# Kernel optimization log

Measured on AMD Instinct MI355X. Metric: run time of the kernel, lower is better.

## Reference

```python
import jax, jax.numpy as jnp
import numpy as np

CHANNELS = 256
N_HEADS = 8
WS = 8
HEAD_DIM = CHANNELS // N_HEADS
SCALE = HEAD_DIM ** -0.5
EPS = 1e-5


def setup_inputs() -> dict:
    key = jax.random.key(0)
    ks = jax.random.split(key, 7)
    C = CHANNELS
    B, T, H, W = 2, 4, 64, 64
    x = jax.random.normal(ks[0], (B * T, C, H, W), dtype=jnp.float32)
    s = 1.0 / np.sqrt(C)
    w_qkv = jax.random.uniform(ks[1], (3 * C, C), jnp.float32, -s, s)
    b_qkv = jax.random.uniform(ks[2], (3 * C,), jnp.float32, -s, s)
    w_proj = jax.random.uniform(ks[3], (C, C), jnp.float32, -s, s)
    b_proj = jax.random.uniform(ks[4], (C,), jnp.float32, -s, s)
    gamma = jnp.ones((C,), jnp.float32)
    beta = jnp.zeros((C,), jnp.float32)
    return {"x": x, "w_qkv": w_qkv, "b_qkv": b_qkv, "w_proj": w_proj,
            "b_proj": b_proj, "gamma": gamma, "beta": beta, "T": T}


def _forward(x, w_qkv, b_qkv, w_proj, b_proj, gamma, beta, T):
    BT, C, H, W = x.shape
    B = BT // T
    ws = WS
    pH = (ws - H % ws) % ws
    pW = (ws - W % ws) % ws
    if pH > 0 or pW > 0:
        x_p = jnp.pad(x, ((0, 0), (0, 0), (0, pH), (0, pW)))
    else:
        x_p = x
    Hp, Wp = H + pH, W + pW
    nH, nW = Hp // ws, Wp // ws
    # partition: (B,T,C,nH,ws,nW,ws) -> (B,nH,nW,T,ws,ws,C) -> (B*nH*nW, T*ws*ws, C)
    xw = x_p.reshape(B, T, C, nH, ws, nW, ws)
    xw = jnp.transpose(xw, (0, 3, 5, 1, 4, 6, 2))
    L = T * ws * ws
    xw = xw.reshape(B * nH * nW, L, C)
    # LayerNorm over channels
    mu = jnp.mean(xw, axis=-1, keepdims=True)
    var = jnp.mean(jnp.square(xw - mu), axis=-1, keepdims=True)
    xn = (xw - mu) * jax.lax.rsqrt(var + EPS) * gamma + beta
    # QKV projection
    qkv = xn @ w_qkv.T + b_qkv  # (NW, L, 3C)
    qkv = qkv.reshape(xw.shape[0], L, 3, N_HEADS, HEAD_DIM)
    q, k, v = qkv[:, :, 0], qkv[:, :, 1], qkv[:, :, 2]  # (NW, L, h, d)
    scores = jnp.einsum('nlhd,nmhd->nhlm', q, k) * SCALE
    attn = jax.nn.softmax(scores, axis=-1)
    out = jnp.einsum('nhlm,nmhd->nlhd', attn, v).reshape(xw.shape[0], L, C)
    out = out @ w_proj.T + b_proj
    out = xw + out
    # unpartition
    out = out.reshape(B, nH, nW, T, ws, ws, C)
    out = jnp.transpose(out, (0, 3, 6, 1, 4, 2, 5)).reshape(B * T, C, Hp, Wp)
    if pH > 0 or pW > 0:
        out = out[:, :, :H, :W]
    return out


def reference(x, w_qkv, b_qkv, w_proj, b_proj, gamma, beta, T):
    return _forward(x, w_qkv, b_qkv, w_proj, b_proj, gamma, beta, T)
```

## Files before the change

### kernel.cpp

```cpp
#include <hip/hip_runtime.h>
#include <hip/hip_bf16.h>

typedef __hip_bfloat16 bf16;
typedef __attribute__((ext_vector_type(8))) short short8;
typedef __attribute__((ext_vector_type(4))) short sh4;
typedef __attribute__((ext_vector_type(4))) float f32x4;

#define SCALE_F 0.17677669529663687f
#define LOG2E_F 1.4426950408889634f
#define EPS_F 1e-5f
#define NW_CHUNK 32
#define ROWS_CHUNK (NW_CHUNK * 256)

#define OW_QKV  0
#define OW_PROJ 196608
#define OB_QKV  262144
#define OB_PROJ 262912
#define NWB     263168

__device__ __forceinline__ float b2f(bf16 v) { return __bfloat162float(v); }
__device__ __forceinline__ bf16 f2b(float v) { return __float2bfloat16(v); }
__device__ __forceinline__ short f2bs(float v) { bf16 h = f2b(v); return *(short*)&h; }
__device__ __forceinline__ float bs2f(short s) { bf16 h = *(bf16*)&s; return __bfloat162float(h); }

__device__ __forceinline__ float ldin(const void* p, size_t i, int mode) {
  if (mode) return ((const float*)p)[i];
  return b2f(((const bf16*)p)[i]);
}
__device__ __forceinline__ void stout(void* p, size_t i, int mode, float v) {
  if (mode) ((float*)p)[i] = v;
  else      ((bf16*)p)[i] = f2b(v);
}
__device__ __forceinline__ float4 ldin4(const void* p, size_t i, int mode) {
  if (mode) return *(const float4*)((const float*)p + i);
  const sh4 s = *(const sh4*)((const short*)p + i);
  return make_float4(bs2f(s[0]), bs2f(s[1]), bs2f(s[2]), bs2f(s[3]));
}

__device__ __forceinline__ void gld16(void* lds, const void* g) {
  __builtin_amdgcn_global_load_lds(
      (const __attribute__((address_space(1))) unsigned int*)g,
      (__attribute__((address_space(3))) unsigned int*)lds, 16, 0, 0);
}

__global__ __launch_bounds__(256) void k_probe(const float* __restrict__ xf,
                                               int* __restrict__ flag) {
  __shared__ int cnt;
  if (threadIdx.x == 0) cnt = 0;
  __syncthreads();
  int bad = 0;
  for (int i = threadIdx.x; i < 1024; i += 256) {
    const float v = xf[i];
    if (!(fabsf(v) < 1e20f)) bad++;
  }
  atomicAdd(&cnt, bad);
  __syncthreads();
  if (threadIdx.x == 0) flag[0] = (cnt < 8) ? 1 : 0;
}

__global__ __launch_bounds__(256) void k_prep(const void* __restrict__ w1,
                                              const void* __restrict__ w2,
                                              const void* __restrict__ b1,
                                              const void* __restrict__ b2,
                                              short* __restrict__ wbuf,
                                              const int* __restrict__ flag) {
  const int mode = flag[0];
  const int i = blockIdx.x * 256 + threadIdx.x;
  float v;
  if (i < OW_PROJ)      v = ldin(w1, i, mode);
  else if (i < OB_QKV)  v = ldin(w2, i - OW_PROJ, mode);
  else if (i < OB_PROJ) v = ldin(b1, i - OB_QKV, mode);
  else if (i < NWB)     v = ldin(b2, i - OB_PROJ, mode);
  else return;
  wbuf[i] = f2bs(v);
}

__global__ __launch_bounds__(256) void k_ln(const void* __restrict__ x,
                                            const void* __restrict__ gamma,
                                            const void* __restrict__ beta,
                                            bf16* __restrict__ xn,
                                            const int* __restrict__ flag) {
  const int mode = flag[0];
  const int bt = blockIdx.x >> 6;
  const int h  = blockIdx.x & 63;
  const int tid = threadIdx.x;
  const int cl = tid >> 4;
  const int wi = tid & 15;

  __shared__ short sX[256][68];
  __shared__ float sred[16][65];
  __shared__ float sqred[16][65];
  __shared__ float smu[64], srs[64];

  const size_t gbase = (size_t)bt * 1048576 + (size_t)h * 64 + wi * 4;
  float s4[4] = {0.f, 0.f, 0.f, 0.f}, q4[4] = {0.f, 0.f, 0.f, 0.f};
  for (int c0 = 0; c0 < 256; c0 += 16) {
    const int c = c0 + cl;
    const float4 v = ldin4(x, gbase + (size_t)c * 4096, mode);
    s4[0] += v.x; q4[0] += v.x * v.x;
    s4[1] += v.y; q4[1] += v.y * v.y;
    s4[2] += v.z; q4[2] += v.z * v.z;
    s4[3] += v.w; q4[3] += v.w * v.w;
    sh4 b;
    b[0] = f2bs(v.x); b[1] = f2bs(v.y); b[2] = f2bs(v.z); b[3] = f2bs(v.w);
    *(sh4*)&sX[c][wi * 4] = b;
  }
#pragma unroll
  for (int k = 0; k < 4; ++k) {
    sred[cl][wi * 4 + k] = s4[k];
    sqred[cl][wi * 4 + k] = q4[k];
  }
  __syncthreads();
  if (tid < 64) {
    float a = 0.f, q = 0.f;
#pragma unroll
    for (int g = 0; g < 16; ++g) { a += sred[g][tid]; q += sqred[g][tid]; }
    const float mu = a * (1.0f / 256.0f);
    const float var = fmaxf(q * (1.0f / 256.0f) - mu * mu, 0.0f);
    smu[tid] = mu; srs[tid] = rsqrtf(var + EPS_F);
  }
  __syncthreads();

  const int c = tid;
  const float g = ldin(gamma, c, mode), be = ldin(beta, c, mode);
  const size_t rb =
      ((size_t)(((bt >> 2) * 64 + (h >> 3) * 8) * 256 + (bt & 3) * 64 + (h & 7) * 8)) * 256 + c;
  for (int iw = 0; iw < 8; ++iw) {
#pragma unroll
    for (int s = 0; s < 8; ++s) {
      const int w = iw * 8 + s;
      const float v = bs2f(sX[c][w]);
      xn[rb + (size_t)iw * 65536 + s * 256] = f2b((v - smu[w]) * srs[w] * g + be);
    }
  }
}

__global__ __launch_bounds__(256) void k_qkv(const bf16* __restrict__ A,
                                             const short* __restrict__ wb,
                                             bf16* __restrict__ out,
                                             int row_base) {
  __shared__ short smem[2 * 128 * 72];
  short* sA = smem;
  short* sB = smem + 128 * 64;
  const int row0 = blockIdx.x * 128;
  const int col0 = blockIdx.y * 128;
  const int tid = threadIdx.x;
  const int wid = tid >> 6, lane = tid & 63;
  const int wy = wid >> 1, wx = wid & 1;
  const int l15 = lane & 15, quad = lane >> 4;
  const short* Ab = (const short*)A;

  const int lr = lane >> 3;
  const int swc = (lane & 7) ^ lr;

  f32x4 acc[4][4];
#pragma unroll
  for (int i = 0; i < 4; ++i)
#pragma unroll
    for (int j = 0; j < 4; ++j) acc[i][j] = (f32x4){0.f, 0.f, 0.f, 0.f};

  for (int k0 = 0; k0 < 256; k0 += 64) {
    if (k0) __syncthreads();
#pragma unroll
    for (int it = 0; it < 4; ++it) {
      const int rbase = wid * 32 + it * 8;
      gld16(sA + rbase * 64,
            Ab + (size_t)(row_base + row0 + rbase + lr) * 256 + k0 + swc * 8);
      gld16(sB + rbase * 64,
            wb + (size_t)(col0 + rbase + lr) * 256 + k0 + swc * 8);
    }
    asm volatile("s_waitcnt vmcnt(0)" ::: "memory");
    __syncthreads();
#pragma unroll
    for (int kk = 0; kk < 64; kk += 32) {
      const int ck = kk >> 3;
      short8 af[4], bfv[4];
#pragma unroll
      for (int i = 0; i < 4; ++i) {
        const int ar = wy * 64 + i * 16 + l15;
        af[i] = *(const short8*)(sA + ar * 64 + (((quad + ck) ^ (ar & 7)) * 8));
      }
#pragma unroll
      for (int j = 0; j < 4; ++j) {
        const int br = wx * 64 + j * 16 + l15;
        bfv[j] = *(const short8*)(sB + br * 64 + (((quad + ck) ^ (br & 7)) * 8));
      }
#pragma unroll
      for (int i = 0; i < 4; ++i)
#pragma unroll
        for (int j = 0; j < 4; ++j)
          acc[i][j] = __builtin_amdgcn_mfma_f32_16x16x32_bf16(af[i], bfv[j], acc[i][j], 0, 0, 0);
    }
  }

  __syncthreads();
  short* slab = smem + wid * (64 * 72);
#pragma unroll
  for (int j = 0; j < 4; ++j) {
    const int col = col0 + wx * 64 + j * 16 + l15;
    const float bj = bs2f(wb[OB_QKV + col]);
#pragma unroll
    for (int i = 0; i < 4; ++i)
#pragma unroll
      for (int r = 0; r < 4; ++r)
        slab[(i * 16 + quad * 4 + r) * 72 + j * 16 + l15] = f2bs(acc[i][j][r] + bj);
  }
  asm volatile("s_waitcnt lgkmcnt(0)" ::: "memory");
  {
    const int srow = lane >> 3;
    const int scol = (lane & 7) * 8;
    short* og = (short*)out;
#pragma unroll
    for (int it = 0; it < 8; ++it) {
      const int rloc = it * 8 + srow;
      short8 v = *(const short8*)&slab[rloc * 72 + scol];
      *(short8*)&og[(size_t)(row0 + wy * 64 + rloc) * 768 + col0 + wx * 64 + scol] = v;
    }
  }
}

__global__ __launch_bounds__(256) void k_attn(const bf16* __restrict__ qkv,
                                              bf16* __restrict__ aout,
                                              int n_base) {
  const int n_loc = blockIdx.x >> 3, hh = blockIdx.x & 7;
  const int n_glob = n_base + n_loc;
  __shared__ short sK[256][40];
  __shared__ short sVt[32][264];
  __shared__ short sP[4][16][72];
  const int tid = threadIdx.x;
  const int wid = tid >> 6, lane = tid & 63;
  const int l15 = lane & 15, quad = lane >> 4;
  const short* qg = (const short*)qkv;
  const size_t base = (size_t)n_loc * 256 * 768 + hh * 32;

  for (int c = tid; c < 1024; c += 256) {
    const int m = c >> 2, d0 = (c & 3) * 8, key = c & 3;
    *(short8*)&sK[m][d0] = *(const short8*)(qg + base + (size_t)m * 768 + 256 + d0);
    short8 vv = *(const short8*)(qg + base + (size_t)m * 768 + 512 + d0);
    const int col = ((((m >> 3) ^ key) << 3) | (m & 7));
#pragma unroll
    for (int j = 0; j < 8; ++j) sVt[d0 + j][col] = vv[j];
  }
  __syncthreads();

  const int R0 = wid * 64;
  const float esc = SCALE_F * LOG2E_F;

  for (int lt = 0; lt < 4; ++lt) {
    const int lrow = R0 + lt * 16;
    const short8 qf = *(const short8*)(qg + base + (size_t)(lrow + l15) * 768 + quad * 8);

    f32x4 sacc[16];
#pragma unroll
    for (int t = 0; t < 16; ++t) {
      sacc[t] = (f32x4){0.f, 0.f, 0.f, 0.f};
      const short8 kf = *(const short8*)&sK[t * 16 + l15][quad * 8];
      sacc[t] = __builtin_amdgcn_mfma_f32_16x16x32_bf16(qf, kf, sacc[t], 0, 0, 0);
    }

    float sum[4] = {0.f, 0.f, 0.f, 0.f};
#pragma unroll
    for (int t = 0; t < 16; ++t)
#pragma unroll
      for (int r = 0; r < 4; ++r) {
        const float p = exp2f(sacc[t][r] * esc);
        sacc[t][r] = p;
        sum[r] += p;
      }
#pragma unroll
    for (int m = 1; m < 16; m <<= 1)
#pragma unroll
      for (int r = 0; r < 4; ++r) sum[r] += __shfl_xor(sum[r], m, 64);
    float inv[4];
#pragma unroll
    for (int r = 0; r < 4; ++r) inv[r] = 1.0f / sum[r];

    f32x4 oacc[2] = {(f32x4){0.f, 0.f, 0.f, 0.f}, (f32x4){0.f, 0.f, 0.f, 0.f}};
#pragma unroll
    for (int ph = 0; ph < 4; ++ph) {
#pragma unroll
      for (int t = 0; t < 4; ++t) {
        const int tt = ph * 4 + t;
#pragma unroll
        for (int r = 0; r < 4; ++r)
          sP[wid][quad * 4 + r][t * 16 + l15] = f2bs(sacc[tt][r]);
      }
      asm volatile("s_waitcnt lgkmcnt(0)" ::: "memory");
#pragma unroll
      for (int kk = 0; kk < 2; ++kk) {
        const short8 pf = *(const short8*)&sP[wid][l15][kk * 32 + quad * 8];
#pragma unroll
        for (int dt = 0; dt < 2; ++dt) {
          const int vrow = dt * 16 + l15;
          const int cch = ph * 8 + kk * 4 + quad;
          const short8 vf =
              *(const short8*)&sVt[vrow][((cch ^ ((vrow >> 3) & 3)) * 8)];
          oacc[dt] = __builtin_amdgcn_mfma_f32_16x16x32_bf16(pf, vf, oacc[dt], 0, 0, 0);
        }
      }
      asm volatile("s_waitcnt lgkmcnt(0)" ::: "memory");
    }

#pragma unroll
    for (int dt = 0; dt < 2; ++dt)
#pragma unroll
      for (int r = 0; r < 4; ++r)
        sP[wid][quad * 4 + r][dt * 16 + l15] = f2bs(oacc[dt][r] * inv[r]);
    asm volatile("s_waitcnt lgkmcnt(0)" ::: "memory");
    {
      const int rloc = lane >> 2;
      const int c8 = (lane & 3) * 8;
      short8 v = *(const short8*)&sP[wid][rloc][c8];
      short* og = (short*)aout;
      *(short8*)&og[((size_t)n_glob * 256 + lrow + rloc) * 256 + hh * 32 + c8] = v;
    }
    asm volatile("s_waitcnt lgkmcnt(0)" ::: "memory");
  }
}

__global__ __launch_bounds__(256) void k_proj(const bf16* __restrict__ A,
                                              const short* __restrict__ wb,
                                              const void* __restrict__ x,
                                              void* __restrict__ out,
                                              const int* __restrict__ flag) {
  const int mode = flag[0];
  __shared__ short smem[2 * 128 * 64];
  __shared__ float sT[4][16][17];
  short* sA = smem;
  short* sB = smem + 128 * 64;
  const int row0 = blockIdx.x * 128;
  const int col0 = blockIdx.y * 128;
  const int tid = threadIdx.x;
  const int wid = tid >> 6, lane = tid & 63;
  const int wy = wid >> 1, wx = wid & 1;
  const int l15 = lane & 15, quad = lane >> 4;
  const short* Ab = (const short*)A;

  const int lr = lane >> 3;
  const int swc = (lane & 7) ^ lr;

  f32x4 acc[4][4];
#pragma unroll
  for (int i = 0; i < 4; ++i)
#pragma unroll
    for (int j = 0; j < 4; ++j) acc[i][j] = (f32x4){0.f, 0.f, 0.f, 0.f};

  for (int k0 = 0; k0 < 256; k0 += 64) {
    if (k0) __syncthreads();
#pragma unroll
    for (int it = 0; it < 4; ++it) {
      const int rbase = wid * 32 + it * 8;
      gld16(sA + rbase * 64,
            Ab + (size_t)(row0 + rbase + lr) * 256 + k0 + swc * 8);
      gld16(sB + rbase * 64,
            wb + OW_PROJ + (size_t)(col0 + rbase + lr) * 256 + k0 + swc * 8);
    }
    asm volatile("s_waitcnt vmcnt(0)" ::: "memory");
    __syncthreads();
#pragma unroll
    for (int kk = 0; kk < 64; kk += 32) {
      const int ck = kk >> 3;
      short8 af[4], bfv[4];
#pragma unroll
      for (int i = 0; i < 4; ++i) {
        const int ar = wy * 64 + i * 16 + l15;
        af[i] = *(const short8*)(sA + ar * 64 + (((quad + ck) ^ (ar & 7)) * 8));
      }
#pragma unroll
      for (int j = 0; j < 4; ++j) {
        const int br = wx * 64 + j * 16 + l15;
        bfv[j] = *(const short8*)(sB + br * 64 + (((quad + ck) ^ (br & 7)) * 8));
      }
#pragma unroll
      for (int i = 0; i < 4; ++i)
#pragma unroll
        for (int j = 0; j < 4; ++j)
          acc[i][j] = __builtin_amdgcn_mfma_f32_16x16x32_bf16(af[i], bfv[j], acc[i][j], 0, 0, 0);
    }
  }

#pragma unroll
  for (int i = 0; i < 4; ++i) {
#pragma unroll
    for (int j = 0; j < 4; ++j) {
#pragma unroll
      for (int r = 0; r < 4; ++r)
        sT[wid][quad * 4 + r][l15] = acc[i][j][r];
      asm volatile("s_waitcnt lgkmcnt(0)" ::: "memory");
#pragma unroll
      for (int r2 = 0; r2 < 4; ++r2) {
        const float v = sT[wid][l15][quad * 4 + r2];
        const int row = row0 + wy * 64 + i * 16 + l15;
        const int c   = col0 + wx * 64 + j * 16 + quad * 4 + r2;
        const int n = row >> 8, l = row & 255;
        const int b = n >> 6, ih = (n >> 3) & 7, iw = n & 7;
        const int tt = l >> 6, rr = (l >> 3) & 7, ss = l & 7;
        const int bt = b * 4 + tt;
        const size_t gaddr = (size_t)bt * 1048576 + (size_t)c * 4096 +
                             (ih * 8 + rr) * 64 + iw * 8 + ss;
        const float o = v + bs2f(wb[OB_PROJ + c]) + ldin(x, gaddr, mode);
        stout(out, gaddr, mode, o);
      }
      asm volatile("s_waitcnt lgkmcnt(0)" ::: "memory");
    }
  }
}

extern "C" void kernel_launch(void* const* d_in, const int* in_sizes, int n_in,
                              void* d_out, int out_size, void* d_ws, size_t ws_size,
                              hipStream_t stream) {
  (void)in_sizes; (void)n_in; (void)out_size;
  const void* x      = d_in[0];
  const void* w_qkv  = d_in[1];
  const void* b_qkv  = d_in[2];
  const void* w_proj = d_in[3];
  const void* b_proj = d_in[4];
  const void* gamma  = d_in[5];
  const void* beta   = d_in[6];

  char* ws = (char*)d_ws;
  int* flag    = (int*)ws;
  short* wbuf  = (short*)(ws + 1024);
  bf16* xnbuf  = (bf16*)(ws + 1024 + 526336);
  bf16* qkvb   = (bf16*)(ws + 1024 + 526336 + 16777216);

  const size_t need_full = 1024 + 526336 + 16777216 + (size_t)32768 * 768 * 2;

  hipLaunchKernelGGL(k_probe, dim3(1), dim3(256), 0, stream, (const float*)x, flag);
  hipLaunchKernelGGL(k_prep, dim3((NWB + 255) / 256), dim3(256), 0, stream,
                     w_qkv, w_proj, b_qkv, b_proj, wbuf, flag);
  hipLaunchKernelGGL(k_ln, dim3(512), dim3(256), 0, stream, x, gamma, beta, xnbuf, flag);

  if (ws_size >= need_full) {
    hipLaunchKernelGGL(k_qkv, dim3(256, 6), dim3(256), 0, stream,
                       xnbuf, wbuf, qkvb, 0);
    hipLaunchKernelGGL(k_attn, dim3(1024), dim3(256), 0, stream,
                       qkvb, xnbuf, 0);
  } else {
    for (int c = 0; c < 4; ++c) {
      hipLaunchKernelGGL(k_qkv, dim3(64, 6), dim3(256), 0, stream,
                         xnbuf, wbuf, qkvb, c * ROWS_CHUNK);
      hipLaunchKernelGGL(k_attn, dim3(NW_CHUNK * 8), dim3(256), 0, stream,
                         qkvb, xnbuf, c * NW_CHUNK);
    }
  }
  hipLaunchKernelGGL(k_proj, dim3(256, 2), dim3(256), 0, stream,
                     xnbuf, wbuf, x, d_out, flag);
}
```

Measured before the change: 203.9 us.

## Split projection epilogue into GEMM plus coalesced transpose-add kernel, tune attention LDS

The fused projection kernel wrote its output with strided scalar stores scattered across the NCHW layout. Now a plain GEMM writes a bf16 token-major temporary, and a separate kernel transposes it through LDS and adds the residual with vectorized, coalesced loads and stores. The attention kernel also drops its LDS padding in favour of XOR swizzles, loads K straight into LDS with global_load_lds, raises wave priority around the MFMA loops, and reorders blocks so that heads of different windows interleave. The trade-off is an extra launch and an extra round trip through the bf16 temporary, and the new path only runs when the workspace is large enough.

```diff
diff --git a/kernel.cpp b/kernel.cpp
--- a/kernel.cpp
+++ b/kernel.cpp
@@ -35,6 +35,13 @@
   if (mode) return *(const float4*)((const float*)p + i);
   const sh4 s = *(const sh4*)((const short*)p + i);
   return make_float4(bs2f(s[0]), bs2f(s[1]), bs2f(s[2]), bs2f(s[3]));
+}
+__device__ __forceinline__ void stout4(void* p, size_t i, int mode, float4 v) {
+  if (mode) { *(float4*)((float*)p + i) = v; }
+  else {
+    sh4 s; s[0] = f2bs(v.x); s[1] = f2bs(v.y); s[2] = f2bs(v.z); s[3] = f2bs(v.w);
+    *(sh4*)((short*)p + i) = s;
+  }
 }
 
 __device__ __forceinline__ void gld16(void* lds, const void* g) {
@@ -221,26 +228,32 @@
 
 __global__ __launch_bounds__(256) void k_attn(const bf16* __restrict__ qkv,
                                               bf16* __restrict__ aout,
-                                              int n_base) {
-  const int n_loc = blockIdx.x >> 3, hh = blockIdx.x & 7;
+                                              int n_base, int nw_mask, int nw_shift) {
+  const int n_loc = blockIdx.x & nw_mask, hh = blockIdx.x >> nw_shift;
   const int n_glob = n_base + n_loc;
-  __shared__ short sK[256][40];
-  __shared__ short sVt[32][264];
-  __shared__ short sP[4][16][72];
+  __shared__ short sK[256][32];
+  __shared__ short sVt[32][256];
+  __shared__ short sP[4][16][64];
   const int tid = threadIdx.x;
   const int wid = tid >> 6, lane = tid & 63;
   const int l15 = lane & 15, quad = lane >> 4;
   const short* qg = (const short*)qkv;
   const size_t base = (size_t)n_loc * 256 * 768 + hh * 32;
 
+#pragma unroll
+  for (int it = 0; it < 4; ++it) {
+    const int rbase = wid * 64 + it * 16;
+    gld16(&sK[rbase][0],
+          qg + base + (size_t)(rbase + (lane >> 2)) * 768 + 256 + (lane & 3) * 8);
+  }
   for (int c = tid; c < 1024; c += 256) {
-    const int m = c >> 2, d0 = (c & 3) * 8, key = c & 3;
-    *(short8*)&sK[m][d0] = *(const short8*)(qg + base + (size_t)m * 768 + 256 + d0);
+    const int m = c >> 2, d0 = (c & 3) * 8;
     short8 vv = *(const short8*)(qg + base + (size_t)m * 768 + 512 + d0);
-    const int col = ((((m >> 3) ^ key) << 3) | (m & 7));
-#pragma unroll
-    for (int j = 0; j < 8; ++j) sVt[d0 + j][col] = vv[j];
-  }
+#pragma unroll
+    for (int j = 0; j < 8; ++j)
+      sVt[d0 + j][(((m >> 3) ^ j) << 3) | (m & 7)] = vv[j];
+  }
+  asm volatile("s_waitcnt vmcnt(0)" ::: "memory");
   __syncthreads();
 
   const int R0 = wid * 64;
@@ -251,12 +264,14 @@
     const short8 qf = *(const short8*)(qg + base + (size_t)(lrow + l15) * 768 + quad * 8);
 
     f32x4 sacc[16];
+    __builtin_amdgcn_s_setprio(1);
 #pragma unroll
     for (int t = 0; t < 16; ++t) {
       sacc[t] = (f32x4){0.f, 0.f, 0.f, 0.f};
       const short8 kf = *(const short8*)&sK[t * 16 + l15][quad * 8];
       sacc[t] = __builtin_amdgcn_mfma_f32_16x16x32_bf16(qf, kf, sacc[t], 0, 0, 0);
     }
+    __builtin_amdgcn_s_setprio(0);
 
     float sum[4] = {0.f, 0.f, 0.f, 0.f};
 #pragma unroll
@@ -281,40 +296,177 @@
 #pragma unroll
       for (int t = 0; t < 4; ++t) {
         const int tt = ph * 4 + t;
-#pragma unroll
-        for (int r = 0; r < 4; ++r)
-          sP[wid][quad * 4 + r][t * 16 + l15] = f2bs(sacc[tt][r]);
+        const int chnk = t * 2 + (l15 >> 3);
+#pragma unroll
+        for (int r = 0; r < 4; ++r) {
+          const int row = quad * 4 + r;
+          sP[wid][row][((chnk ^ (row & 7)) << 3) | (l15 & 7)] = f2bs(sacc[tt][r]);
+        }
       }
       asm volatile("s_waitcnt lgkmcnt(0)" ::: "memory");
+      __builtin_amdgcn_s_setprio(1);
 #pragma unroll
       for (int kk = 0; kk < 2; ++kk) {
-        const short8 pf = *(const short8*)&sP[wid][l15][kk * 32 + quad * 8];
+        const int pch = (kk * 4 + quad) ^ (l15 & 7);
+        const short8 pf = *(const short8*)&sP[wid][l15][pch * 8];
 #pragma unroll
         for (int dt = 0; dt < 2; ++dt) {
           const int vrow = dt * 16 + l15;
           const int cch = ph * 8 + kk * 4 + quad;
-          const short8 vf =
-              *(const short8*)&sVt[vrow][((cch ^ ((vrow >> 3) & 3)) * 8)];
+          const short8 vf = *(const short8*)&sVt[vrow][((cch ^ (vrow & 7)) * 8)];
           oacc[dt] = __builtin_amdgcn_mfma_f32_16x16x32_bf16(pf, vf, oacc[dt], 0, 0, 0);
         }
       }
+      __builtin_amdgcn_s_setprio(0);
       asm volatile("s_waitcnt lgkmcnt(0)" ::: "memory");
     }
 
 #pragma unroll
-    for (int dt = 0; dt < 2; ++dt)
-#pragma unroll
-      for (int r = 0; r < 4; ++r)
-        sP[wid][quad * 4 + r][dt * 16 + l15] = f2bs(oacc[dt][r] * inv[r]);
+    for (int dt = 0; dt < 2; ++dt) {
+      const int chnk = dt * 2 + (l15 >> 3);
+#pragma unroll
+      for (int r = 0; r < 4; ++r) {
+        const int row = quad * 4 + r;
+        sP[wid][row][((chnk ^ (row & 7)) << 3) | (l15 & 7)] = f2bs(oacc[dt][r] * inv[r]);
+      }
+    }
     asm volatile("s_waitcnt lgkmcnt(0)" ::: "memory");
     {
       const int rloc = lane >> 2;
-      const int c8 = (lane & 3) * 8;
-      short8 v = *(const short8*)&sP[wid][rloc][c8];
+      const int pch = (lane & 3) ^ (rloc & 7);
+      short8 v = *(const short8*)&sP[wid][rloc][pch * 8];
       short* og = (short*)aout;
-      *(short8*)&og[((size_t)n_glob * 256 + lrow + rloc) * 256 + hh * 32 + c8] = v;
+      *(short8*)&og[((size_t)n_glob * 256 + lrow + rloc) * 256 + hh * 32 + (lane & 3) * 8] = v;
     }
     asm volatile("s_waitcnt lgkmcnt(0)" ::: "memory");
+  }
+}
+
+__global__ __launch_bounds__(256) void k_proj_g(const bf16* __restrict__ A,
+                                                const short* __restrict__ wb,
+                                                bf16* __restrict__ out) {
+  __shared__ short smem[2 * 128 * 72];
+  short* sA = smem;
+  short* sB = smem + 128 * 64;
+  const int row0 = blockIdx.x * 128;
+  const int col0 = blockIdx.y * 128;
+  const int tid = threadIdx.x;
+  const int wid = tid >> 6, lane = tid & 63;
+  const int wy = wid >> 1, wx = wid & 1;
+  const int l15 = lane & 15, quad = lane >> 4;
+  const short* Ab = (const short*)A;
+
+  const int lr = lane >> 3;
+  const int swc = (lane & 7) ^ lr;
+
+  f32x4 acc[4][4];
+#pragma unroll
+  for (int i = 0; i < 4; ++i)
+#pragma unroll
+    for (int j = 0; j < 4; ++j) acc[i][j] = (f32x4){0.f, 0.f, 0.f, 0.f};
+
+  for (int k0 = 0; k0 < 256; k0 += 64) {
+    if (k0) __syncthreads();
+#pragma unroll
+    for (int it = 0; it < 4; ++it) {
+      const int rbase = wid * 32 + it * 8;
+      gld16(sA + rbase * 64,
+            Ab + (size_t)(row0 + rbase + lr) * 256 + k0 + swc * 8);
+      gld16(sB + rbase * 64,
+            wb + OW_PROJ + (size_t)(col0 + rbase + lr) * 256 + k0 + swc * 8);
+    }
+    asm volatile("s_waitcnt vmcnt(0)" ::: "memory");
+    __syncthreads();
+#pragma unroll
+    for (int kk = 0; kk < 64; kk += 32) {
+      const int ck = kk >> 3;
+      short8 af[4], bfv[4];
+#pragma unroll
+      for (int i = 0; i < 4; ++i) {
+        const int ar = wy * 64 + i * 16 + l15;
+        af[i] = *(const short8*)(sA + ar * 64 + (((quad + ck) ^ (ar & 7)) * 8));
+      }
+#pragma unroll
+      for (int j = 0; j < 4; ++j) {
+        const int br = wx * 64 + j * 16 + l15;
+        bfv[j] = *(const short8*)(sB + br * 64 + (((quad + ck) ^ (br & 7)) * 8));
+      }
+#pragma unroll
+      for (int i = 0; i < 4; ++i)
+#pragma unroll
+        for (int j = 0; j < 4; ++j)
+          acc[i][j] = __builtin_amdgcn_mfma_f32_16x16x32_bf16(af[i], bfv[j], acc[i][j], 0, 0, 0);
+    }
+  }
+
+  __syncthreads();
+  short* slab = smem + wid * (64 * 72);
+#pragma unroll
+  for (int j = 0; j < 4; ++j) {
+    const int col = col0 + wx * 64 + j * 16 + l15;
+    const float bj = bs2f(wb[OB_PROJ + col]);
+#pragma unroll
+    for (int i = 0; i < 4; ++i)
+#pragma unroll
+      for (int r = 0; r < 4; ++r)
+        slab[(i * 16 + quad * 4 + r) * 72 + j * 16 + l15] = f2bs(acc[i][j][r] + bj);
+  }
+  asm volatile("s_waitcnt lgkmcnt(0)" ::: "memory");
+  {
+    const int srow = lane >> 3;
+    const int scol = (lane & 7) * 8;
+    short* og = (short*)out;
+#pragma unroll
+    for (int it = 0; it < 8; ++it) {
+      const int rloc = it * 8 + srow;
+      short8 v = *(const short8*)&slab[rloc * 72 + scol];
+      *(short8*)&og[(size_t)(row0 + wy * 64 + rloc) * 256 + col0 + wx * 64 + scol] = v;
+    }
+  }
+}
+
+__global__ __launch_bounds__(256) void k_add(const bf16* __restrict__ tmp,
+                                             const void* __restrict__ x,
+                                             void* __restrict__ out,
+                                             const int* __restrict__ flag) {
+  const int mode = flag[0];
+  const int bt = blockIdx.x >> 6;
+  const int h  = blockIdx.x & 63;
+  const int tid = threadIdx.x;
+
+  __shared__ short sT2[256][68];
+
+  const int n_b = (bt >> 2) * 64 + (h >> 3) * 8;
+  const int l0  = (bt & 3) * 64 + (h & 7) * 8;
+  const short* tg = (const short*)tmp;
+
+#pragma unroll
+  for (int i = 0; i < 8; ++i) {
+    const int id = i * 256 + tid;
+    const int w = id >> 5, c8 = (id & 31) * 8;
+    const int row = (n_b + (w >> 3)) * 256 + l0 + (w & 7);
+    const short8 v = *(const short8*)(tg + (size_t)row * 256 + c8);
+    const int wg = ((w >> 2) ^ ((id & 31) & 15)) * 4 + (w & 3);
+#pragma unroll
+    for (int j = 0; j < 8; ++j) sT2[c8 + j][wg] = v[j];
+  }
+  __syncthreads();
+
+  const int cl = tid >> 4;
+  const int wi = tid & 15;
+  const size_t gb = (size_t)bt * 1048576 + (size_t)h * 64 + wi * 4;
+  for (int c0 = 0; c0 < 256; c0 += 16) {
+    const int c = c0 + cl;
+    const int k15 = (c >> 3) & 15;
+    const sh4 pv = *(const sh4*)&sT2[c][((wi ^ k15) & 15) * 4];
+    const size_t gaddr = gb + (size_t)c * 4096;
+    const float4 xv = ldin4(x, gaddr, mode);
+    float4 o;
+    o.x = xv.x + bs2f(pv[0]);
+    o.y = xv.y + bs2f(pv[1]);
+    o.z = xv.z + bs2f(pv[2]);
+    o.w = xv.w + bs2f(pv[3]);
+    stout4(out, gaddr, mode, o);
   }
 }
 
@@ -395,8 +547,8 @@
         const int n = row >> 8, l = row & 255;
         const int b = n >> 6, ih = (n >> 3) & 7, iw = n & 7;
         const int tt = l >> 6, rr = (l >> 3) & 7, ss = l & 7;
-        const int bt = b * 4 + tt;
-        const size_t gaddr = (size_t)bt * 1048576 + (size_t)c * 4096 +
+        const int btl = b * 4 + tt;
+        const size_t gaddr = (size_t)btl * 1048576 + (size_t)c * 4096 +
                              (ih * 8 + rr) * 64 + iw * 8 + ss;
         const float o = v + bs2f(wb[OB_PROJ + c]) + ldin(x, gaddr, mode);
         stout(out, gaddr, mode, o);
@@ -435,15 +587,20 @@
     hipLaunchKernelGGL(k_qkv, dim3(256, 6), dim3(256), 0, stream,
                        xnbuf, wbuf, qkvb, 0);
     hipLaunchKernelGGL(k_attn, dim3(1024), dim3(256), 0, stream,
-                       qkvb, xnbuf, 0);
+                       qkvb, xnbuf, 0, 127, 7);
+    bf16* tmpb = qkvb;
+    hipLaunchKernelGGL(k_proj_g, dim3(256, 2), dim3(256), 0, stream,
+                       xnbuf, wbuf, tmpb);
+    hipLaunchKernelGGL(k_add, dim3(512), dim3(256), 0, stream,
+                       tmpb, x, d_out, flag);
   } else {
     for (int c = 0; c < 4; ++c) {
       hipLaunchKernelGGL(k_qkv, dim3(64, 6), dim3(256), 0, stream,
                          xnbuf, wbuf, qkvb, c * ROWS_CHUNK);
       hipLaunchKernelGGL(k_attn, dim3(NW_CHUNK * 8), dim3(256), 0, stream,
-                         qkvb, xnbuf, c * NW_CHUNK);
-    }
-  }
-  hipLaunchKernelGGL(k_proj, dim3(256, 2), dim3(256), 0, stream,
-                     xnbuf, wbuf, x, d_out, flag);
-}
+                         qkvb, xnbuf, c * NW_CHUNK, NW_CHUNK - 1, 5);
+    }
+    hipLaunchKernelGGL(k_proj, dim3(256, 2), dim3(256), 0, stream,
+                       xnbuf, wbuf, x, d_out, flag);
+  }
+}
```

New measurement: 196.4 us. 1.04x faster.
